# Performance work log

Measured on AMD Instinct MI355X. Metric: run time of the kernel, lower is better.

## Reference

```python
import jax, jax.numpy as jnp
import numpy as np

L, N, E = 2048, 2, 512
H = 8
HD = E // H
FF = 2048
NLAYERS = 2
EPS = 1e-5


def setup_inputs() -> dict:
    key = jax.random.key(0)
    ks = jax.random.split(key, 8)
    s = 0.02
    return {
        "src": jax.random.normal(ks[0], (L, N, E), jnp.float32),
        # packed qkv projection, torch Linear convention: y = x @ W.T + b
        "in_proj_w": jax.random.normal(ks[1], (NLAYERS, 3 * E, E), jnp.float32) * s,
        "in_proj_b": jnp.zeros((NLAYERS, 3 * E), jnp.float32),
        "out_proj_w": jax.random.normal(ks[2], (NLAYERS, E, E), jnp.float32) * s,
        "out_proj_b": jnp.zeros((NLAYERS, E), jnp.float32),
        "lin1_w": jax.random.normal(ks[3], (NLAYERS, FF, E), jnp.float32) * s,
        "lin1_b": jnp.zeros((NLAYERS, FF), jnp.float32),
        "lin2_w": jax.random.normal(ks[4], (NLAYERS, E, FF), jnp.float32) * s,
        "lin2_b": jnp.zeros((NLAYERS, E), jnp.float32),
        "ln1_g": jnp.ones((NLAYERS, E), jnp.float32),
        "ln1_b": jnp.zeros((NLAYERS, E), jnp.float32),
        "ln2_g": jnp.ones((NLAYERS, E), jnp.float32),
        "ln2_b": jnp.zeros((NLAYERS, E), jnp.float32),
    }


def _layer_norm(x, g, b):
    mu = jnp.mean(x, axis=-1, keepdims=True)
    var = jnp.mean(jnp.square(x - mu), axis=-1, keepdims=True)
    return (x - mu) * jax.lax.rsqrt(var + EPS) * g + b


def _mha(x, w_qkv, b_qkv, w_o, b_o):
    # x: [L, N, E] (seq-first, as in torch multi_head_attention_forward)
    qkv = jnp.einsum('lne,fe->lnf', x, w_qkv) + b_qkv  # [L, N, 3E]
    q, k, v = jnp.split(qkv, 3, axis=-1)
    q = q.reshape(L, N, H, HD) * (1.0 / np.sqrt(HD))  # torch scales q pre-bmm
    k = k.reshape(L, N, H, HD)
    v = v.reshape(L, N, H, HD)
    scores = jnp.einsum('lnhd,snhd->nhls', q, k)  # [N, H, L, S] -- O(L*S) matrix
    attn = jax.nn.softmax(scores, axis=-1)
    o = jnp.einsum('nhls,snhd->lnhd', attn, v).reshape(L, N, E)
    return jnp.einsum('lne,fe->lnf', o, w_o) + b_o


def reference(src, in_proj_w, in_proj_b, out_proj_w, out_proj_b,
              lin1_w, lin1_b, lin2_w, lin2_b, ln1_g, ln1_b, ln2_g, ln2_b):
    x = src
    for i in range(NLAYERS):  # fixed small layer count
        a = _mha(x, in_proj_w[i], in_proj_b[i], out_proj_w[i], out_proj_b[i])
        x = _layer_norm(x + a, ln1_g[i], ln1_b[i])  # post-norm (torch default)
        h = jax.nn.relu(jnp.einsum('lne,fe->lnf', x, lin1_w[i]) + lin1_b[i])
        f = jnp.einsum('lnf,ef->lne', h, lin2_w[i]) + lin2_b[i]
        x = _layer_norm(x + f, ln2_g[i], ln2_b[i])
    return x
```

## Files before the change

### kernel.cpp

```cpp
#include <hip/hip_runtime.h>
#include <hip/hip_bf16.h>

using bf16 = __hip_bfloat16;
typedef __bf16 bf16x8 __attribute__((ext_vector_type(8)));
typedef float f32x4 __attribute__((ext_vector_type(4)));

#define MFMA(a, b, c) __builtin_amdgcn_mfma_f32_16x16x32_bf16(a, b, c, 0, 0, 0)

constexpr int L = 2048, N = 2, E = 512, H = 8, HD = 64, FF = 2048;
constexpr int T = L * N;

__global__ void detect_dtype(const unsigned int* __restrict__ g,
                             int* __restrict__ flag) {
  if (threadIdx.x == 0 && blockIdx.x == 0)
    *flag = (g[0] != 0x3F800000u) ? 1 : 0;
}

__global__ __launch_bounds__(256) void cvt_to_bf16(
    const void* __restrict__ in, bf16* __restrict__ out, int n,
    const int* __restrict__ flag) {
  int i = (blockIdx.x * 256 + threadIdx.x) * 8;
  if (i >= n) return;
  if (*flag) {
    *(uint4*)&out[i] = *(const uint4*)&((const bf16*)in)[i];
  } else {
    float4 a = *(const float4*)&((const float*)in)[i];
    float4 b = *(const float4*)&((const float*)in)[i + 4];
    bf16 o8[8] = {__float2bfloat16(a.x), __float2bfloat16(a.y),
                  __float2bfloat16(a.z), __float2bfloat16(a.w),
                  __float2bfloat16(b.x), __float2bfloat16(b.y),
                  __float2bfloat16(b.z), __float2bfloat16(b.w)};
    *(uint4*)&out[i] = *(const uint4*)o8;
  }
}

__global__ __launch_bounds__(256) void cvt_to_f32(
    const void* __restrict__ in, float* __restrict__ out, int n,
    const int* __restrict__ flag) {
  int i = blockIdx.x * 256 + threadIdx.x;
  if (i >= n) return;
  out[i] = (*flag) ? __bfloat162float(((const bf16*)in)[i])
                   : ((const float*)in)[i];
}

__device__ __forceinline__ void gload16(const bf16* g, bf16* l) {
  __builtin_amdgcn_global_load_lds(
      (const __attribute__((address_space(1))) unsigned int*)g,
      (__attribute__((address_space(3))) unsigned int*)l, 16, 0, 0);
}

template <bool RELU, int BN>
__global__ __launch_bounds__(256) void gemm_pipe(
    const bf16* __restrict__ A, const bf16* __restrict__ W,
    const float* __restrict__ bias, bf16* __restrict__ C,
    int M, int F, int K) {
  constexpr int D = 4;
  constexpr int GB = BN / 64;
  constexpr int FN = BN / 32;
  __shared__ __align__(16) bf16 As[D][128 * 32];
  __shared__ __align__(16) bf16 Bs[D][BN * 32];
  const int bm = blockIdx.x, bn = blockIdx.y;
  const int tid = threadIdx.x;
  const int w = tid >> 6, lane = tid & 63;
  const int wr = w >> 1, wc = w & 1;
  const int lhi = lane >> 4, llo = lane & 15;
  f32x4 acc[4][FN] = {};

  const bf16 *ap[2], *wp[GB];
#pragma unroll
  for (int s = 0; s < 2; ++s) {
    int c = tid + s * 256;
    ap[s] = &A[(size_t)(bm * 128 + (c >> 2)) * K + (c & 3) * 8];
  }
#pragma unroll
  for (int s = 0; s < GB; ++s) {
    int c = tid + s * 256;
    wp[s] = &W[(size_t)(bn * BN + (c >> 2)) * K + (c & 3) * 8];
  }
  auto stage = [&](int buf, int k0) {
#pragma unroll
    for (int s = 0; s < 2; ++s)
      gload16(ap[s] + k0, &As[buf][(tid + s * 256) * 8]);
#pragma unroll
    for (int s = 0; s < GB; ++s)
      gload16(wp[s] + k0, &Bs[buf][(tid + s * 256) * 8]);
  };

  const int nsteps = K / 32;
  stage(0, 0);
  stage(1, 32);
  stage(2, 64);

  for (int t = 0; t < nsteps; ++t) {
    const int cur = t & 3;
    if (t < nsteps - 2) {
      if constexpr (BN == 128)
        asm volatile("s_waitcnt vmcnt(8)" ::: "memory");
      else
        asm volatile("s_waitcnt vmcnt(6)" ::: "memory");
    } else if (t == nsteps - 2) {
      if constexpr (BN == 128)
        asm volatile("s_waitcnt vmcnt(4)" ::: "memory");
      else
        asm volatile("s_waitcnt vmcnt(3)" ::: "memory");
    } else {
      asm volatile("s_waitcnt vmcnt(0)" ::: "memory");
    }
    __builtin_amdgcn_s_barrier();
    asm volatile("" ::: "memory");
    __builtin_amdgcn_sched_barrier(0);
    if (t + 3 < nsteps) stage((t + 3) & 3, (t + 3) * 32);

    bf16x8 af[4], bfr[FN];
#pragma unroll
    for (int mi = 0; mi < 4; ++mi)
      af[mi] =
          *(const bf16x8*)&As[cur][(wr * 64 + mi * 16 + llo) * 32 + lhi * 8];
#pragma unroll
    for (int ni = 0; ni < FN; ++ni)
      bfr[ni] = *(const bf16x8*)&Bs[cur]
          [(wc * (FN * 16) + ni * 16 + llo) * 32 + lhi * 8];
    __builtin_amdgcn_s_setprio(1);
#pragma unroll
    for (int mi = 0; mi < 4; ++mi)
#pragma unroll
      for (int ni = 0; ni < FN; ++ni)
        acc[mi][ni] = MFMA(af[mi], bfr[ni], acc[mi][ni]);
    __builtin_amdgcn_s_setprio(0);
  }
#pragma unroll
  for (int mi = 0; mi < 4; ++mi) {
#pragma unroll
    for (int ni = 0; ni < FN; ++ni) {
      int col = bn * BN + wc * (FN * 16) + ni * 16 + llo;
      float bv = bias[col];
#pragma unroll
      for (int r = 0; r < 4; ++r) {
        int row = bm * 128 + wr * 64 + mi * 16 + lhi * 4 + r;
        float v = acc[mi][ni][r] + bv;
        if (RELU) v = fmaxf(v, 0.f);
        C[(size_t)row * F + col] = __float2bfloat16(v);
      }
    }
  }
}

__global__ __launch_bounds__(256) void prep_kv(
    const bf16* __restrict__ qkv, bf16* __restrict__ kt,
    bf16* __restrict__ vt) {
  __shared__ __align__(16) bf16 Vl[64 * 72];
  const int blk = blockIdx.x;
  const int kb = blk & 31, nh = blk >> 5;
  const int n = nh >> 3, h = nh & 7;
  const int tid = threadIdx.x;
  bf16* ko = kt + ((size_t)nh * 32 + kb) * 4096;
  bf16* vo = vt + ((size_t)nh * 32 + kb) * 4096;
#pragma unroll
  for (int s = 0; s < 2; ++s) {
    int c = tid + s * 256;
    int jj = c >> 3, g = c & 7;
    size_t t = (size_t)((kb * 64 + jj) * N + n);
    uint4 kk = *(const uint4*)&qkv[t * 1536 + 512 + h * 64 + g * 8];
    *(uint4*)&ko[jj * 64 + ((g ^ (jj & 7)) * 8)] = kk;
    uint4 vv = *(const uint4*)&qkv[t * 1536 + 1024 + h * 64 + g * 8];
    *(uint4*)&Vl[jj * 72 + g * 8] = vv;
  }
  __syncthreads();
#pragma unroll
  for (int s = 0; s < 2; ++s) {
    int c = tid + s * 256;
    int d = c >> 3, gsw = c & 7;
    int g = gsw ^ (d & 7);
    bf16 tmp[8];
#pragma unroll
    for (int e = 0; e < 8; ++e) tmp[e] = Vl[(g * 8 + e) * 72 + d];
    *(uint4*)&vo[d * 64 + gsw * 8] = *(const uint4*)tmp;
  }
}

__global__ __launch_bounds__(256) void attn_split(
    const bf16* __restrict__ qkv, const bf16* __restrict__ kt,
    const bf16* __restrict__ vt, bf16* __restrict__ opart,
    float* __restrict__ lpart) {
  __shared__ __align__(16) bf16 Kb[2][4096];
  __shared__ __align__(16) bf16 Vb[2][4096];
  __shared__ __align__(16) bf16 Ps[64 * 72];
  const int blk = blockIdx.x;
  const int qb = blk & 31;
  const int nh = (blk >> 5) & 15;
  const int split = blk >> 9;
  const int n = nh >> 3, h = nh & 7;
  const int tid = threadIdx.x;
  const int w = tid >> 6, lane = tid & 63;
  const int lhi = lane >> 4, llo = lane & 15;
  const int kb0 = split * 8, kb1 = kb0 + 8;

#pragma unroll
  for (int s = 0; s < 2; ++s) {
    int c = tid + s * 256;
    int i = c >> 3, dc = c & 7;
    size_t t = (size_t)((qb * 64 + i) * N + n);
    *(uint4*)&Ps[i * 72 + dc * 8] =
        *(const uint4*)&qkv[t * 1536 + h * 64 + dc * 8];
  }
  __syncthreads();
  bf16x8 aq[2];
  aq[0] = *(const bf16x8*)&Ps[(w * 16 + llo) * 72 + 0 + lhi * 8];
  aq[1] = *(const bf16x8*)&Ps[(w * 16 + llo) * 72 + 32 + lhi * 8];

  const bf16* ktile = kt + (size_t)nh * 32 * 4096;
  const bf16* vtile = vt + (size_t)nh * 32 * 4096;
  auto stage = [&](int buf, int kb) {
#pragma unroll
    for (int s = 0; s < 2; ++s) {
      int c = tid + s * 256;
      gload16(ktile + (size_t)kb * 4096 + c * 8, &Kb[buf][c * 8]);
      gload16(vtile + (size_t)kb * 4096 + c * 8, &Vb[buf][c * 8]);
    }
  };
  stage(0, kb0);

  float psum[4] = {0.f, 0.f, 0.f, 0.f};
  f32x4 o[4] = {};
  int cur = 0;

  for (int kb = kb0; kb < kb1; ++kb) {
    __syncthreads();
    if (kb + 1 < kb1) stage(cur ^ 1, kb + 1);

    f32x4 sfr[4] = {};
    __builtin_amdgcn_s_setprio(1);
#pragma unroll
    for (int cb = 0; cb < 4; ++cb) {
      const int row = cb * 16 + llo;
#pragma unroll
      for (int ks = 0; ks < 2; ++ks) {
        bf16x8 b = *(const bf16x8*)&Kb[cur]
            [row * 64 + (((ks * 4 + lhi) ^ (row & 7)) << 3)];
        sfr[cb] = MFMA(aq[ks], b, sfr[cb]);
      }
    }
    __builtin_amdgcn_s_setprio(0);

#pragma unroll
    for (int cb = 0; cb < 4; ++cb) {
#pragma unroll
      for (int r = 0; r < 4; ++r) {
        float p = __expf(sfr[cb][r] * 0.125f);
        psum[r] += p;
        Ps[(w * 16 + lhi * 4 + r) * 72 + cb * 16 + llo] = __float2bfloat16(p);
      }
    }
    asm volatile("" ::: "memory");

    __builtin_amdgcn_s_setprio(1);
#pragma unroll
    for (int cb = 0; cb < 4; ++cb) {
      const int crow = cb * 16 + llo;
#pragma unroll
      for (int ks = 0; ks < 2; ++ks) {
        bf16x8 a =
            *(const bf16x8*)&Ps[(w * 16 + llo) * 72 + ks * 32 + lhi * 8];
        bf16x8 b = *(const bf16x8*)&Vb[cur]
            [crow * 64 + (((ks * 4 + lhi) ^ (crow & 7)) << 3)];
        o[cb] = MFMA(a, b, o[cb]);
      }
    }
    __builtin_amdgcn_s_setprio(0);
    cur ^= 1;
  }

#pragma unroll
  for (int r = 0; r < 4; ++r) {
    float v = psum[r];
#pragma unroll
    for (int d = 1; d < 16; d <<= 1) v += __shfl_xor(v, d);
    psum[r] = v;
  }
#pragma unroll
  for (int cb = 0; cb < 4; ++cb) {
#pragma unroll
    for (int r = 0; r < 4; ++r) {
      int i = w * 16 + lhi * 4 + r;
      int d = cb * 16 + llo;
      size_t t = (size_t)((qb * 64 + i) * N + n);
      opart[((size_t)split * T + t) * E + h * 64 + d] =
          __float2bfloat16(o[cb][r]);
    }
  }
  if (llo == 0) {
#pragma unroll
    for (int r = 0; r < 4; ++r) {
      int i = w * 16 + lhi * 4 + r;
      size_t t = (size_t)((qb * 64 + i) * N + n);
      lpart[(size_t)(split * T + t) * H + h] = psum[r];
    }
  }
}

__global__ __launch_bounds__(256) void attn_merge(
    const bf16* __restrict__ opart, const float* __restrict__ lpart,
    bf16* __restrict__ atn) {
  int i = (blockIdx.x * 256 + threadIdx.x) * 8;
  if (i >= T * E) return;
  int t = i >> 9, h = (i >> 6) & 7;
  float l = 0.f, acc[8] = {};
#pragma unroll
  for (int s = 0; s < 4; ++s) {
    l += lpart[(size_t)(s * T + t) * H + h];
    uint4 v = *(const uint4*)&opart[(size_t)s * T * E + i];
    const bf16* e8 = (const bf16*)&v;
#pragma unroll
    for (int e = 0; e < 8; ++e) acc[e] += __bfloat162float(e8[e]);
  }
  float rl = 1.f / l;
  bf16 r8[8];
#pragma unroll
  for (int e = 0; e < 8; ++e) r8[e] = __float2bfloat16(acc[e] * rl);
  *(uint4*)&atn[i] = *(const uint4*)r8;
}

template <typename OutT>
__global__ __launch_bounds__(256) void add_ln(
    const bf16* __restrict__ res, const bf16* __restrict__ y,
    const float* __restrict__ g, const float* __restrict__ b,
    OutT* __restrict__ out) {
  const int t = blockIdx.x;
  const int tid = threadIdx.x;
  const int w = tid >> 6, lane = tid & 63;
  const int e = tid * 2;
  const size_t base = (size_t)t * E;
  float v0 = __bfloat162float(res[base + e]) + __bfloat162float(y[base + e]);
  float v1 = __bfloat162float(res[base + e + 1]) + __bfloat162float(y[base + e + 1]);
  float s = v0 + v1, q = v0 * v0 + v1 * v1;
#pragma unroll
  for (int d = 1; d < 64; d <<= 1) {
    s += __shfl_xor(s, d);
    q += __shfl_xor(q, d);
  }
  __shared__ float rs[4], rq[4];
  if (lane == 0) { rs[w] = s; rq[w] = q; }
  __syncthreads();
  float S = rs[0] + rs[1] + rs[2] + rs[3];
  float Qq = rq[0] + rq[1] + rq[2] + rq[3];
  float mu = S * (1.f / E);
  float var = Qq * (1.f / E) - mu * mu;
  float rstd = rsqrtf(var + 1e-5f);
  float o0 = (v0 - mu) * rstd * g[e] + b[e];
  float o1 = (v1 - mu) * rstd * g[e + 1] + b[e + 1];
  if constexpr (__is_same(OutT, float)) {
    out[base + e] = o0;
    out[base + e + 1] = o1;
  } else {
    out[base + e] = __float2bfloat16(o0);
    out[base + e + 1] = __float2bfloat16(o1);
  }
}

extern "C" void kernel_launch(void* const* d_in, const int* in_sizes, int n_in,
                              void* d_out, int out_size, void* d_ws,
                              size_t ws_size, hipStream_t stream) {
  int* flag = (int*)d_ws;
  float* pbuf = (float*)((char*)d_ws + 16);
  float* in_b = pbuf;
  float* ob   = in_b + 3072;
  float* l1b  = ob + 1024;
  float* l2b  = l1b + 4096;
  float* ln1g = l2b + 1024;
  float* ln1b = ln1g + 1024;
  float* ln2g = ln1b + 1024;
  float* ln2b = ln2g + 1024;
  bf16* big  = (bf16*)(ln2b + 1024);
  bf16* srcb = big;
  bf16* in_w = srcb + (size_t)T * E;
  bf16* ow   = in_w + (size_t)2 * 1536 * E;
  bf16* l1w  = ow + (size_t)2 * E * E;
  bf16* l2w  = l1w + (size_t)2 * FF * E;
  bf16* qkv  = l2w + (size_t)2 * E * FF;
  bf16* atn  = qkv + (size_t)T * 1536;
  bf16* ybuf = atn + (size_t)T * E;
  bf16* x1   = ybuf + (size_t)T * E;
  bf16* x2   = x1 + (size_t)T * E;
  bf16* hbuf = x2 + (size_t)T * E;
  bf16* ktg  = hbuf + (size_t)T * FF;
  bf16* vtg  = ktg + (size_t)T * E;
  bf16* opart  = hbuf;
  float* lpart = (float*)ybuf;

  detect_dtype<<<1, 64, 0, stream>>>((const unsigned int*)d_in[9], flag);
  auto cvtb = [&](const void* in, bf16* out, int n) {
    cvt_to_bf16<<<dim3(n / 2048), 256, 0, stream>>>(in, out, n, flag);
  };
  auto cvtf = [&](const void* in, float* out, int n) {
    cvt_to_f32<<<dim3(n / 256), 256, 0, stream>>>(in, out, n, flag);
  };
  cvtb(d_in[0], srcb, T * E);
  cvtb(d_in[1], in_w, 2 * 1536 * E);
  cvtb(d_in[3], ow, 2 * E * E);
  cvtb(d_in[5], l1w, 2 * FF * E);
  cvtb(d_in[7], l2w, 2 * E * FF);
  cvtf(d_in[2], in_b, 3072);
  cvtf(d_in[4], ob, 1024);
  cvtf(d_in[6], l1b, 4096);
  cvtf(d_in[8], l2b, 1024);
  cvtf(d_in[9], ln1g, 1024);
  cvtf(d_in[10], ln1b, 1024);
  cvtf(d_in[11], ln2g, 1024);
  cvtf(d_in[12], ln2b, 1024);

  const bf16* x = srcb;
  for (int i = 0; i < 2; ++i) {
    gemm_pipe<false, 128><<<dim3(T / 128, 1536 / 128), 256, 0, stream>>>(
        x, in_w + (size_t)i * 1536 * E, in_b + i * 1536, qkv, T, 1536, E);
    prep_kv<<<dim3(512), 256, 0, stream>>>(qkv, ktg, vtg);
    attn_split<<<dim3(2048), 256, 0, stream>>>(qkv, ktg, vtg, opart, lpart);
    attn_merge<<<dim3(T * E / 2048), 256, 0, stream>>>(opart, lpart, atn);
    gemm_pipe<false, 64><<<dim3(T / 128, E / 64), 256, 0, stream>>>(
        atn, ow + (size_t)i * E * E, ob + i * E, ybuf, T, E, E);
    add_ln<bf16><<<dim3(T), 256, 0, stream>>>(
        x, ybuf, ln1g + i * E, ln1b + i * E, x1);
    gemm_pipe<true, 128><<<dim3(T / 128, FF / 128), 256, 0, stream>>>(
        x1, l1w + (size_t)i * FF * E, l1b + i * FF, hbuf, T, FF, E);
    gemm_pipe<false, 64><<<dim3(T / 128, E / 64), 256, 0, stream>>>(
        hbuf, l2w + (size_t)i * E * FF, l2b + i * E, ybuf, T, E, FF);
    if (i == 1) {
      add_ln<float><<<dim3(T), 256, 0, stream>>>(
          x1, ybuf, ln2g + i * E, ln2b + i * E, (float*)d_out);
    } else {
      add_ln<bf16><<<dim3(T), 256, 0, stream>>>(
          x1, ybuf, ln2g + i * E, ln2b + i * E, x2);
    }
    x = x2;
  }
}
```

Measured before the change: 337.6 us.

## Replace 4-stage GEMM pipeline with double-buffered K=64 k-major tiled GEMM

Replaces the 4-deep global_load_lds pipeline (K-step 32, hand-tuned vmcnt waits) with a simpler double-buffered loop that uses K-step 64. Shared tiles are now stored k-group-major, which changes the LDS access pattern for fragment reads. The out-projection and FFN-down GEMMs switch from 128x64 to 64x64 tiles to launch more blocks. In exchange the loop waits on a full __syncthreads each step with less prefetch depth, which may expose more load latency.

```diff
diff --git a/kernel.cpp b/kernel.cpp
--- a/kernel.cpp
+++ b/kernel.cpp
@@ -49,94 +49,84 @@
       (__attribute__((address_space(3))) unsigned int*)l, 16, 0, 0);
 }
 
-template <bool RELU, int BN>
-__global__ __launch_bounds__(256) void gemm_pipe(
+template <bool RELU, int BM, int BN>
+__global__ __launch_bounds__(256) void gemm_bt(
     const bf16* __restrict__ A, const bf16* __restrict__ W,
     const float* __restrict__ bias, bf16* __restrict__ C,
     int M, int F, int K) {
-  constexpr int D = 4;
-  constexpr int GB = BN / 64;
-  constexpr int FN = BN / 32;
-  __shared__ __align__(16) bf16 As[D][128 * 32];
-  __shared__ __align__(16) bf16 Bs[D][BN * 32];
+  constexpr int SA = BM / 32;
+  constexpr int SB = BN / 32;
+  constexpr int MI = BM / 32;
+  constexpr int NI = BN / 32;
+  __shared__ __align__(16) bf16 As[2][BM * 64];
+  __shared__ __align__(16) bf16 Bs[2][BN * 64];
   const int bm = blockIdx.x, bn = blockIdx.y;
   const int tid = threadIdx.x;
   const int w = tid >> 6, lane = tid & 63;
   const int wr = w >> 1, wc = w & 1;
   const int lhi = lane >> 4, llo = lane & 15;
-  f32x4 acc[4][FN] = {};
-
-  const bf16 *ap[2], *wp[GB];
-#pragma unroll
-  for (int s = 0; s < 2; ++s) {
+  f32x4 acc[MI][NI] = {};
+
+  const bf16 *ap[SA], *wp[SB];
+#pragma unroll
+  for (int s = 0; s < SA; ++s) {
     int c = tid + s * 256;
-    ap[s] = &A[(size_t)(bm * 128 + (c >> 2)) * K + (c & 3) * 8];
-  }
-#pragma unroll
-  for (int s = 0; s < GB; ++s) {
+    int kg = c / BM, row = c % BM;
+    ap[s] = &A[(size_t)(bm * BM + row) * K + kg * 8];
+  }
+#pragma unroll
+  for (int s = 0; s < SB; ++s) {
     int c = tid + s * 256;
-    wp[s] = &W[(size_t)(bn * BN + (c >> 2)) * K + (c & 3) * 8];
+    int kg = c / BN, row = c % BN;
+    wp[s] = &W[(size_t)(bn * BN + row) * K + kg * 8];
   }
   auto stage = [&](int buf, int k0) {
 #pragma unroll
-    for (int s = 0; s < 2; ++s)
+    for (int s = 0; s < SA; ++s)
       gload16(ap[s] + k0, &As[buf][(tid + s * 256) * 8]);
 #pragma unroll
-    for (int s = 0; s < GB; ++s)
+    for (int s = 0; s < SB; ++s)
       gload16(wp[s] + k0, &Bs[buf][(tid + s * 256) * 8]);
   };
 
-  const int nsteps = K / 32;
   stage(0, 0);
-  stage(1, 32);
-  stage(2, 64);
-
-  for (int t = 0; t < nsteps; ++t) {
-    const int cur = t & 3;
-    if (t < nsteps - 2) {
-      if constexpr (BN == 128)
-        asm volatile("s_waitcnt vmcnt(8)" ::: "memory");
-      else
-        asm volatile("s_waitcnt vmcnt(6)" ::: "memory");
-    } else if (t == nsteps - 2) {
-      if constexpr (BN == 128)
-        asm volatile("s_waitcnt vmcnt(4)" ::: "memory");
-      else
-        asm volatile("s_waitcnt vmcnt(3)" ::: "memory");
-    } else {
-      asm volatile("s_waitcnt vmcnt(0)" ::: "memory");
-    }
-    __builtin_amdgcn_s_barrier();
-    asm volatile("" ::: "memory");
-    __builtin_amdgcn_sched_barrier(0);
-    if (t + 3 < nsteps) stage((t + 3) & 3, (t + 3) * 32);
-
-    bf16x8 af[4], bfr[FN];
-#pragma unroll
-    for (int mi = 0; mi < 4; ++mi)
-      af[mi] =
-          *(const bf16x8*)&As[cur][(wr * 64 + mi * 16 + llo) * 32 + lhi * 8];
-#pragma unroll
-    for (int ni = 0; ni < FN; ++ni)
-      bfr[ni] = *(const bf16x8*)&Bs[cur]
-          [(wc * (FN * 16) + ni * 16 + llo) * 32 + lhi * 8];
+  int cur = 0;
+  for (int k0 = 0; k0 < K; k0 += 64) {
+    __syncthreads();
+    if (k0 + 64 < K) stage(cur ^ 1, k0 + 64);
+    bf16x8 af[MI][2], bfr[NI][2];
+#pragma unroll
+    for (int mi = 0; mi < MI; ++mi)
+#pragma unroll
+      for (int ks = 0; ks < 2; ++ks)
+        af[mi][ks] = *(const bf16x8*)&As[cur]
+            [((ks * 4 + lhi) * BM + wr * (BM / 2) + mi * 16 + llo) * 8];
+#pragma unroll
+    for (int ni = 0; ni < NI; ++ni)
+#pragma unroll
+      for (int ks = 0; ks < 2; ++ks)
+        bfr[ni][ks] = *(const bf16x8*)&Bs[cur]
+            [((ks * 4 + lhi) * BN + wc * (BN / 2) + ni * 16 + llo) * 8];
     __builtin_amdgcn_s_setprio(1);
 #pragma unroll
-    for (int mi = 0; mi < 4; ++mi)
-#pragma unroll
-      for (int ni = 0; ni < FN; ++ni)
-        acc[mi][ni] = MFMA(af[mi], bfr[ni], acc[mi][ni]);
+    for (int ks = 0; ks < 2; ++ks)
+#pragma unroll
+      for (int mi = 0; mi < MI; ++mi)
+#pragma unroll
+        for (int ni = 0; ni < NI; ++ni)
+          acc[mi][ni] = MFMA(af[mi][ks], bfr[ni][ks], acc[mi][ni]);
     __builtin_amdgcn_s_setprio(0);
-  }
-#pragma unroll
-  for (int mi = 0; mi < 4; ++mi) {
-#pragma unroll
-    for (int ni = 0; ni < FN; ++ni) {
-      int col = bn * BN + wc * (FN * 16) + ni * 16 + llo;
+    cur ^= 1;
+  }
+#pragma unroll
+  for (int mi = 0; mi < MI; ++mi) {
+#pragma unroll
+    for (int ni = 0; ni < NI; ++ni) {
+      int col = bn * BN + wc * (BN / 2) + ni * 16 + llo;
       float bv = bias[col];
 #pragma unroll
       for (int r = 0; r < 4; ++r) {
-        int row = bm * 128 + wr * 64 + mi * 16 + lhi * 4 + r;
+        int row = bm * BM + wr * (BM / 2) + mi * 16 + lhi * 4 + r;
         float v = acc[mi][ni][r] + bv;
         if (RELU) v = fmaxf(v, 0.f);
         C[(size_t)row * F + col] = __float2bfloat16(v);
@@ -410,18 +400,18 @@
 
   const bf16* x = srcb;
   for (int i = 0; i < 2; ++i) {
-    gemm_pipe<false, 128><<<dim3(T / 128, 1536 / 128), 256, 0, stream>>>(
+    gemm_bt<false, 128, 128><<<dim3(T / 128, 1536 / 128), 256, 0, stream>>>(
         x, in_w + (size_t)i * 1536 * E, in_b + i * 1536, qkv, T, 1536, E);
     prep_kv<<<dim3(512), 256, 0, stream>>>(qkv, ktg, vtg);
     attn_split<<<dim3(2048), 256, 0, stream>>>(qkv, ktg, vtg, opart, lpart);
     attn_merge<<<dim3(T * E / 2048), 256, 0, stream>>>(opart, lpart, atn);
-    gemm_pipe<false, 64><<<dim3(T / 128, E / 64), 256, 0, stream>>>(
+    gemm_bt<false, 64, 64><<<dim3(T / 64, E / 64), 256, 0, stream>>>(
         atn, ow + (size_t)i * E * E, ob + i * E, ybuf, T, E, E);
     add_ln<bf16><<<dim3(T), 256, 0, stream>>>(
         x, ybuf, ln1g + i * E, ln1b + i * E, x1);
-    gemm_pipe<true, 128><<<dim3(T / 128, FF / 128), 256, 0, stream>>>(
+    gemm_bt<true, 128, 128><<<dim3(T / 128, FF / 128), 256, 0, stream>>>(
         x1, l1w + (size_t)i * FF * E, l1b + i * FF, hbuf, T, FF, E);
-    gemm_pipe<false, 64><<<dim3(T / 128, E / 64), 256, 0, stream>>>(
+    gemm_bt<false, 64, 64><<<dim3(T / 64, E / 64), 256, 0, stream>>>(
         hbuf, l2w + (size_t)i * E * FF, l2b + i * E, ybuf, T, E, FF);
     if (i == 1) {
       add_ln<float><<<dim3(T), 256, 0, stream>>>(
```

New measurement: 330.4 us. 1.02x faster.
